# Performance work log

Hardware: AMD Instinct MI355X
Metric: run time of the kernel (lower is better)

The kernel has to match this reference:

```python
import jax, jax.numpy as jnp
import numpy as np
import math

B, C, H = 1, 3, 224
EPS = 0.05
P_INIT = 0.8
N_QUERIES = 5000


def _p_selection(it):
    # static python schedule (rescale_schedule=False)
    if 10 < it <= 50:
        return P_INIT / 2
    elif 50 < it <= 200:
        return P_INIT / 4
    elif 200 < it <= 500:
        return P_INIT / 8
    elif 500 < it <= 1000:
        return P_INIT / 16
    elif 1000 < it <= 2000:
        return P_INIT / 32
    elif 2000 < it <= 4000:
        return P_INIT / 64
    elif 4000 < it <= 6000:
        return P_INIT / 128
    elif 6000 < it <= 8000:
        return P_INIT / 256
    elif 8000 < it:
        return P_INIT / 512
    return P_INIT


def _s_schedule():
    # patch side length per iteration; pure python -> static array
    n_features = C * H * H
    return np.array(
        [max(int(round(math.sqrt(_p_selection(i) * n_features / C))), 1) for i in range(N_QUERIES)],
        dtype=np.int32,
    )


def setup_inputs() -> dict:
    key = jax.random.key(0)
    x = jax.random.uniform(key, (B, C, H, H), dtype=jnp.float32)  # image in [0,1]
    return {"x": x}


def _forward(x):
    base = jax.random.key(1)
    # init: vertical-stripe random-sign perturbation, shape [B, C, 1, H]
    k0 = jax.random.fold_in(base, 0)
    init_sign = jnp.sign(2.0 * jax.random.uniform(k0, (x.shape[0], C, 1, H), dtype=x.dtype) - 1.0)
    x_best = jnp.clip(x + EPS * init_sign, 0.0, 1.0)

    x_lo = x - EPS
    x_hi = x + EPS
    s_arr = jnp.asarray(_s_schedule())  # [N_QUERIES] int32
    idx = jnp.arange(H)

    def step(xb, si):
        s, i = si
        k = jax.random.fold_in(base, i + 1)
        k1, k2 = jax.random.split(k)
        # vh = floor(uniform * (H - s)) in {0, ..., H-s-1}
        u = jax.random.uniform(k1, (), dtype=x.dtype)
        vh = jnp.floor(u * (H - s).astype(x.dtype)).astype(jnp.int32)
        # per-channel random sign, constant over the s x s patch
        sgn = jnp.sign(2.0 * jax.random.uniform(k2, (C, 1, 1), dtype=x.dtype) - 1.0)
        # square patch mask [H, H] at offset vh with side s (mask instead of
        # dynamic-size slice assignment; jit-friendly)
        m = (idx >= vh) & (idx < vh + s)
        mask = (m[:, None] & m[None, :]).astype(x.dtype)
        xb = xb + 2.0 * EPS * sgn * mask            # broadcasts to [B, C, H, H]
        xb = jnp.clip(jnp.minimum(jnp.maximum(xb, x_lo), x_hi), 0.0, 1.0)
        return xb, None

    x_best, _ = jax.lax.scan(step, x_best, (s_arr, jnp.arange(N_QUERIES)))
    return x_best


def reference(x):
    return _forward(x)
```

## Files before the change

kernel.cpp:

```cpp
#include <hip/hip_runtime.h>
#include <stdint.h>


#define HH 224
#define NQ 5000
#define NPIX (HH * HH)
#define EPSF 0.05f

__device__ __forceinline__ void tf2x32(uint32_t k0, uint32_t k1,
                                       uint32_t x0, uint32_t x1,
                                       uint32_t& o0, uint32_t& o1) {
  uint32_t ks2 = k0 ^ k1 ^ 0x1BD11BDAu;
  x0 += k0; x1 += k1;
#define TFR(r) { x0 += x1; x1 = (x1 << (r)) | (x1 >> (32 - (r))); x1 ^= x0; }
  TFR(13) TFR(15) TFR(26) TFR(6)
  x0 += k1;  x1 += ks2 + 1u;
  TFR(17) TFR(29) TFR(16) TFR(24)
  x0 += ks2; x1 += k0 + 2u;
  TFR(13) TFR(15) TFR(26) TFR(6)
  x0 += k0;  x1 += k1 + 3u;
  TFR(17) TFR(29) TFR(16) TFR(24)
  x0 += k1;  x1 += ks2 + 4u;
  TFR(13) TFR(15) TFR(26) TFR(6)
  x0 += ks2; x1 += k0 + 5u;
#undef TFR
  o0 = x0; o1 = x1;
}

__device__ __forceinline__ int sign_from_bits(uint32_t bits) {
  uint32_t mant = bits >> 9;
  return (mant > 0x400000u) ? 1 : ((mant < 0x400000u) ? -1 : 0);
}

__device__ __forceinline__ float u01_from_bits(uint32_t bits) {
  return __uint_as_float(0x3f800000u | (bits >> 9)) - 1.0f;
}

__constant__ int SEG_LO_C[8] = {0, 11, 51, 201, 501, 1001, 2001, 4001};
__constant__ int SEG_HI_C[8] = {10, 50, 200, 500, 1000, 2000, 4000, 4999};
__constant__ int SEG_SZ_C[8] = {200, 142, 100, 71, 50, 35, 25, 18};

__global__ __launch_bounds__(512) void build_kernel(uint16_t* __restrict__ gtab,
                                                    int8_t* __restrict__ gisign) {
  int blk = blockIdx.x;
  int tid = threadIdx.x;

  if (blk == 24) {
    uint32_t g0, g1;
    tf2x32(0u, 1u, 0u, 0u, g0, g1);
    for (int i = tid; i < 3 * HH; i += 512) {
      uint32_t o0, o1;
      tf2x32(g0, g1, 0u, (uint32_t)i, o0, o1);
      gisign[i] = (int8_t)sign_from_bits(o0 ^ o1);
    }
    return;
  }

  int seg = blk / 3, c = blk % 3;
  int s = SEG_SZ_C[seg];
  __shared__ uint32_t bins[224];
  __shared__ uint16_t tab[8 * 224];
  if (tid < 224) bins[tid] = 0;
  __syncthreads();

  for (int t = SEG_LO_C[seg] + tid; t <= SEG_HI_C[seg]; t += 512) {
    uint32_t f0, f1;
    tf2x32(0u, 1u, 0u, (uint32_t)(t + 1), f0, f1);
    uint32_t a0, a1, b0, b1;
    tf2x32(f0, f1, 0u, 0u, a0, a1);
    tf2x32(f0, f1, 0u, 1u, b0, b1);
    uint32_t u0, u1;
    tf2x32(a0, a1, 0u, 0u, u0, u1);
    int vh = (int)floorf(u01_from_bits(u0 ^ u1) * (float)(HH - s));
    uint32_t c0, c1;
    tf2x32(b0, b1, 0u, (uint32_t)c, c0, c1);
    int g = sign_from_bits(c0 ^ c1);
    if (g) atomicMax(&bins[vh], (((uint32_t)(t + 1)) << 1) | (uint32_t)(g > 0));
  }
  __syncthreads();

  if (tid < 224) tab[tid] = (uint16_t)bins[tid];
  __syncthreads();
  for (int k = 1; k < 8; ++k) {
    int w = 1 << (k - 1);
    if (tid < 224) {
      uint16_t a = tab[(k - 1) * 224 + tid];
      uint16_t b = (tid + w < 224) ? tab[(k - 1) * 224 + tid + w] : (uint16_t)0;
      tab[k * 224 + tid] = (a > b) ? a : b;
    }
    __syncthreads();
  }

  const uint32_t* t32 = (const uint32_t*)tab;
  uint32_t* g32 = (uint32_t*)(gtab + (seg * 3 + c) * 1792);
  for (int i = tid; i < 896; i += 512) g32[i] = t32[i];
}

__global__ __launch_bounds__(256) void resolve_kernel(const uint16_t* __restrict__ gtab,
                                                      const int8_t* __restrict__ isign,
                                                      const float* __restrict__ x,
                                                      float* __restrict__ out) {
  int c = blockIdx.y;
  int p = blockIdx.x * 256 + threadIdx.x;
  int pi = p / HH, pj = p % HH;
  int m = min(pi, pj), M = max(pi, pj);

  const uint16_t* tc = gtab + c * 1792;

  const int SEG_S[8] = {200, 142, 100, 71, 50, 35, 25, 18};
  uint32_t best = 0;
#pragma unroll
  for (int seg = 0; seg < 8; ++seg) {
    const int s = SEG_S[seg];
    int lo = max(0, M - s + 1);
    int hi = min(m, 223 - s);
    bool ok = (lo <= hi);
    int len = ok ? (hi - lo + 1) : 1;
    int k = 31 - __clz(len);
    int o2 = hi + 1 - (1 << k);
    int b = seg * 5376 + k * 224;
    uint32_t v = max((uint32_t)tc[b + lo], (uint32_t)tc[b + o2]);
    best = max(best, ok ? v : 0u);
  }

  int sg = best ? ((best & 1u) ? 1 : -1) : (int)isign[c * HH + pj];

  int idx = c * NPIX + p;
  float xv = x[idx];
  out[idx] = (sg > 0) ? fminf(xv + EPSF, 1.0f)
           : (sg < 0) ? fmaxf(xv - EPSF, 0.0f)
                      : fminf(fmaxf(xv, 0.0f), 1.0f);
}

extern "C" void kernel_launch(void* const* d_in, const int* in_sizes, int n_in,
                              void* d_out, int out_size, void* d_ws, size_t ws_size,
                              hipStream_t stream) {
  const float* x = (const float*)d_in[0];
  float* out = (float*)d_out;
  uint16_t* gtab = (uint16_t*)d_ws;
  int8_t* gisign = (int8_t*)d_ws + 86016;

  build_kernel<<<25, 512, 0, stream>>>(gtab, gisign);
  dim3 rgrid(NPIX / 256, 3);
  resolve_kernel<<<rgrid, 256, 0, stream>>>(gtab, gisign, x, out);
}
```

Baseline: 66.09 us.

## Fuse table build and resolve into one kernel with per-block recomputation

Merges the RNG-driven table build and the per-pixel resolve into a single kernel, where every block recomputes all 5000 query draws for its channel into shared-memory bins and sparse tables. This removes the second launch, the global workspace round trip and the cross-kernel dependency. In exchange each block does the full RNG loop redundantly (about 10 serial passes per thread instead of at most 4), and uses larger shared memory, which lengthens the per-block critical path.

```diff
diff --git a/kernel.cpp b/kernel.cpp
--- a/kernel.cpp
+++ b/kernel.cpp
@@ -36,34 +36,32 @@
   return __uint_as_float(0x3f800000u | (bits >> 9)) - 1.0f;
 }
 
-__constant__ int SEG_LO_C[8] = {0, 11, 51, 201, 501, 1001, 2001, 4001};
-__constant__ int SEG_HI_C[8] = {10, 50, 200, 500, 1000, 2000, 4000, 4999};
+__device__ __forceinline__ int seg_of(int t) {
+  if (t <= 10)   return 0;
+  if (t <= 50)   return 1;
+  if (t <= 200)  return 2;
+  if (t <= 500)  return 3;
+  if (t <= 1000) return 4;
+  if (t <= 2000) return 5;
+  if (t <= 4000) return 6;
+  return 7;
+}
 __constant__ int SEG_SZ_C[8] = {200, 142, 100, 71, 50, 35, 25, 18};
 
-__global__ __launch_bounds__(512) void build_kernel(uint16_t* __restrict__ gtab,
-                                                    int8_t* __restrict__ gisign) {
+__global__ __launch_bounds__(512) void fused_kernel(const float* __restrict__ x,
+                                                    float* __restrict__ out) {
+  __shared__ uint32_t bins[8 * 224];
+  __shared__ uint16_t tab[8 * 8 * 224];
+  __shared__ int8_t isign_l[224];
   int blk = blockIdx.x;
   int tid = threadIdx.x;
+  int c = blk / 98;
+  int p = (blk - c * 98) * 512 + tid;
 
-  if (blk == 24) {
-    uint32_t g0, g1;
-    tf2x32(0u, 1u, 0u, 0u, g0, g1);
-    for (int i = tid; i < 3 * HH; i += 512) {
-      uint32_t o0, o1;
-      tf2x32(g0, g1, 0u, (uint32_t)i, o0, o1);
-      gisign[i] = (int8_t)sign_from_bits(o0 ^ o1);
-    }
-    return;
-  }
-
-  int seg = blk / 3, c = blk % 3;
-  int s = SEG_SZ_C[seg];
-  __shared__ uint32_t bins[224];
-  __shared__ uint16_t tab[8 * 224];
-  if (tid < 224) bins[tid] = 0;
+  for (int i = tid; i < 8 * 224; i += 512) bins[i] = 0;
   __syncthreads();
 
-  for (int t = SEG_LO_C[seg] + tid; t <= SEG_HI_C[seg]; t += 512) {
+  for (int t = tid; t < NQ; t += 512) {
     uint32_t f0, f1;
     tf2x32(0u, 1u, 0u, (uint32_t)(t + 1), f0, f1);
     uint32_t a0, a1, b0, b1;
@@ -71,41 +69,43 @@
     tf2x32(f0, f1, 0u, 1u, b0, b1);
     uint32_t u0, u1;
     tf2x32(a0, a1, 0u, 0u, u0, u1);
+    int seg = seg_of(t);
+    int s = SEG_SZ_C[seg];
     int vh = (int)floorf(u01_from_bits(u0 ^ u1) * (float)(HH - s));
     uint32_t c0, c1;
     tf2x32(b0, b1, 0u, (uint32_t)c, c0, c1);
     int g = sign_from_bits(c0 ^ c1);
-    if (g) atomicMax(&bins[vh], (((uint32_t)(t + 1)) << 1) | (uint32_t)(g > 0));
+    if (g) atomicMax(&bins[seg * 224 + vh],
+                     (((uint32_t)(t + 1)) << 1) | (uint32_t)(g > 0));
+  }
+
+  if (tid < 224) {
+    uint32_t g0, g1;
+    tf2x32(0u, 1u, 0u, 0u, g0, g1);
+    uint32_t o0, o1;
+    tf2x32(g0, g1, 0u, (uint32_t)(c * 224 + tid), o0, o1);
+    isign_l[tid] = (int8_t)sign_from_bits(o0 ^ o1);
   }
   __syncthreads();
 
-  if (tid < 224) tab[tid] = (uint16_t)bins[tid];
+  for (int i = tid; i < 8 * 224; i += 512) {
+    int seg = i / 224, v = i % 224;
+    tab[(seg * 8) * 224 + v] = (uint16_t)bins[i];
+  }
   __syncthreads();
   for (int k = 1; k < 8; ++k) {
     int w = 1 << (k - 1);
-    if (tid < 224) {
-      uint16_t a = tab[(k - 1) * 224 + tid];
-      uint16_t b = (tid + w < 224) ? tab[(k - 1) * 224 + tid + w] : (uint16_t)0;
-      tab[k * 224 + tid] = (a > b) ? a : b;
+    for (int i = tid; i < 8 * 224; i += 512) {
+      int seg = i / 224, v = i % 224;
+      uint16_t a = tab[(seg * 8 + k - 1) * 224 + v];
+      uint16_t b = (v + w < 224) ? tab[(seg * 8 + k - 1) * 224 + v + w] : (uint16_t)0;
+      tab[(seg * 8 + k) * 224 + v] = (a > b) ? a : b;
     }
     __syncthreads();
   }
 
-  const uint32_t* t32 = (const uint32_t*)tab;
-  uint32_t* g32 = (uint32_t*)(gtab + (seg * 3 + c) * 1792);
-  for (int i = tid; i < 896; i += 512) g32[i] = t32[i];
-}
-
-__global__ __launch_bounds__(256) void resolve_kernel(const uint16_t* __restrict__ gtab,
-                                                      const int8_t* __restrict__ isign,
-                                                      const float* __restrict__ x,
-                                                      float* __restrict__ out) {
-  int c = blockIdx.y;
-  int p = blockIdx.x * 256 + threadIdx.x;
   int pi = p / HH, pj = p % HH;
   int m = min(pi, pj), M = max(pi, pj);
-
-  const uint16_t* tc = gtab + c * 1792;
 
   const int SEG_S[8] = {200, 142, 100, 71, 50, 35, 25, 18};
   uint32_t best = 0;
@@ -118,12 +118,12 @@
     int len = ok ? (hi - lo + 1) : 1;
     int k = 31 - __clz(len);
     int o2 = hi + 1 - (1 << k);
-    int b = seg * 5376 + k * 224;
-    uint32_t v = max((uint32_t)tc[b + lo], (uint32_t)tc[b + o2]);
+    int b = (seg * 8 + k) * 224;
+    uint32_t v = max((uint32_t)tab[b + lo], (uint32_t)tab[b + o2]);
     best = max(best, ok ? v : 0u);
   }
 
-  int sg = best ? ((best & 1u) ? 1 : -1) : (int)isign[c * HH + pj];
+  int sg = best ? ((best & 1u) ? 1 : -1) : (int)isign_l[pj];
 
   int idx = c * NPIX + p;
   float xv = x[idx];
@@ -137,10 +137,5 @@
                               hipStream_t stream) {
   const float* x = (const float*)d_in[0];
   float* out = (float*)d_out;
-  uint16_t* gtab = (uint16_t*)d_ws;
-  int8_t* gisign = (int8_t*)d_ws + 86016;
-
-  build_kernel<<<25, 512, 0, stream>>>(gtab, gisign);
-  dim3 rgrid(NPIX / 256, 3);
-  resolve_kernel<<<rgrid, 256, 0, stream>>>(gtab, gisign, x, out);
+  fused_kernel<<<294, 512, 0, stream>>>(x, out);
 }
```

Result: slower. 109.7 us (+66.0%).

## Fuse table build and resolve into one kernel with flag-based spin wait

Applied to the files above, without the earlier changes.

Merges the two launches into a single 294-block kernel. The first 24 blocks build the sparse max tables and publish completion through release-stored magic flags. Every block prefetches its pixel and computes the init sign inline, then thread 0 spins on the 24 flags before the table lookups, which use atomic loads. This removes the second launch and the gap between the kernels. In exchange it depends on all blocks being resident at once, and the flags are never cleared, so later calls may not wait for the rebuilt tables.

```diff
diff --git a/kernel.cpp b/kernel.cpp
--- a/kernel.cpp
+++ b/kernel.cpp
@@ -6,6 +6,7 @@
 #define NQ 5000
 #define NPIX (HH * HH)
 #define EPSF 0.05f
+#define MAGIC 0x5EED0000u
 
 __device__ __forceinline__ void tf2x32(uint32_t k0, uint32_t k1,
                                        uint32_t x0, uint32_t x1,
@@ -40,72 +41,88 @@
 __constant__ int SEG_HI_C[8] = {10, 50, 200, 500, 1000, 2000, 4000, 4999};
 __constant__ int SEG_SZ_C[8] = {200, 142, 100, 71, 50, 35, 25, 18};
 
-__global__ __launch_bounds__(512) void build_kernel(uint16_t* __restrict__ gtab,
-                                                    int8_t* __restrict__ gisign) {
+__global__ __launch_bounds__(512) void spin_fused(const float* __restrict__ x,
+                                                  float* __restrict__ out,
+                                                  uint16_t* __restrict__ gtab,
+                                                  uint32_t* __restrict__ flags) {
+  __shared__ uint32_t bins[224];
+  __shared__ uint16_t tab[8 * 224];
+  __shared__ int ready;
   int blk = blockIdx.x;
   int tid = threadIdx.x;
 
-  if (blk == 24) {
-    uint32_t g0, g1;
-    tf2x32(0u, 1u, 0u, 0u, g0, g1);
-    for (int i = tid; i < 3 * HH; i += 512) {
-      uint32_t o0, o1;
-      tf2x32(g0, g1, 0u, (uint32_t)i, o0, o1);
-      gisign[i] = (int8_t)sign_from_bits(o0 ^ o1);
+  if (blk < 24) {
+    int seg = blk / 3, c = blk % 3;
+    int s = SEG_SZ_C[seg];
+    if (tid < 224) bins[tid] = 0;
+    __syncthreads();
+    for (int t = SEG_LO_C[seg] + tid; t <= SEG_HI_C[seg]; t += 512) {
+      uint32_t f0, f1;
+      tf2x32(0u, 1u, 0u, (uint32_t)(t + 1), f0, f1);
+      uint32_t a0, a1, b0, b1;
+      tf2x32(f0, f1, 0u, 0u, a0, a1);
+      tf2x32(f0, f1, 0u, 1u, b0, b1);
+      uint32_t u0, u1;
+      tf2x32(a0, a1, 0u, 0u, u0, u1);
+      int vh = (int)floorf(u01_from_bits(u0 ^ u1) * (float)(HH - s));
+      uint32_t c0, c1;
+      tf2x32(b0, b1, 0u, (uint32_t)c, c0, c1);
+      int g = sign_from_bits(c0 ^ c1);
+      if (g) atomicMax(&bins[vh], (((uint32_t)(t + 1)) << 1) | (uint32_t)(g > 0));
     }
-    return;
+    __syncthreads();
+    if (tid < 224) tab[tid] = (uint16_t)bins[tid];
+    __syncthreads();
+    for (int k = 1; k < 8; ++k) {
+      int w = 1 << (k - 1);
+      if (tid < 224) {
+        uint16_t a = tab[(k - 1) * 224 + tid];
+        uint16_t b = (tid + w < 224) ? tab[(k - 1) * 224 + tid + w] : (uint16_t)0;
+        tab[k * 224 + tid] = (a > b) ? a : b;
+      }
+      __syncthreads();
+    }
+    const uint32_t* t32 = (const uint32_t*)tab;
+    uint32_t* g32 = (uint32_t*)(gtab + (seg * 3 + c) * 1792);
+    for (int i = tid; i < 896; i += 512) g32[i] = t32[i];
+    __threadfence();
+    __syncthreads();
+    if (tid == 0)
+      __hip_atomic_store(&flags[blk], MAGIC + (uint32_t)blk,
+                         __ATOMIC_RELEASE, __HIP_MEMORY_SCOPE_AGENT);
   }
 
-  int seg = blk / 3, c = blk % 3;
-  int s = SEG_SZ_C[seg];
-  __shared__ uint32_t bins[224];
-  __shared__ uint16_t tab[8 * 224];
-  if (tid < 224) bins[tid] = 0;
-  __syncthreads();
+  int c = blk / 98;
+  int p = (blk - c * 98) * 512 + tid;
+  int gid = c * NPIX + p;
+  float xv = x[gid];
 
-  for (int t = SEG_LO_C[seg] + tid; t <= SEG_HI_C[seg]; t += 512) {
-    uint32_t f0, f1;
-    tf2x32(0u, 1u, 0u, (uint32_t)(t + 1), f0, f1);
-    uint32_t a0, a1, b0, b1;
-    tf2x32(f0, f1, 0u, 0u, a0, a1);
-    tf2x32(f0, f1, 0u, 1u, b0, b1);
-    uint32_t u0, u1;
-    tf2x32(a0, a1, 0u, 0u, u0, u1);
-    int vh = (int)floorf(u01_from_bits(u0 ^ u1) * (float)(HH - s));
-    uint32_t c0, c1;
-    tf2x32(b0, b1, 0u, (uint32_t)c, c0, c1);
-    int g = sign_from_bits(c0 ^ c1);
-    if (g) atomicMax(&bins[vh], (((uint32_t)(t + 1)) << 1) | (uint32_t)(g > 0));
+  int pj = p % HH;
+  int isg;
+  {
+    uint32_t g0, g1, o0, o1;
+    tf2x32(0u, 1u, 0u, 0u, g0, g1);
+    tf2x32(g0, g1, 0u, (uint32_t)(c * HH + pj), o0, o1);
+    isg = sign_from_bits(o0 ^ o1);
+  }
+
+  if (tid == 0) {
+    int good = 0;
+    for (int it = 0; it < (1 << 22) && good < 24; ++it) {
+      good = 0;
+      for (int i = 0; i < 24; ++i)
+        good += (__hip_atomic_load(&flags[i], __ATOMIC_ACQUIRE,
+                                   __HIP_MEMORY_SCOPE_AGENT) == MAGIC + (uint32_t)i);
+      if (good < 24) __builtin_amdgcn_s_sleep(8);
+    }
+    ready = 1;
   }
   __syncthreads();
+  (void)ready;
 
-  if (tid < 224) tab[tid] = (uint16_t)bins[tid];
-  __syncthreads();
-  for (int k = 1; k < 8; ++k) {
-    int w = 1 << (k - 1);
-    if (tid < 224) {
-      uint16_t a = tab[(k - 1) * 224 + tid];
-      uint16_t b = (tid + w < 224) ? tab[(k - 1) * 224 + tid + w] : (uint16_t)0;
-      tab[k * 224 + tid] = (a > b) ? a : b;
-    }
-    __syncthreads();
-  }
-
-  const uint32_t* t32 = (const uint32_t*)tab;
-  uint32_t* g32 = (uint32_t*)(gtab + (seg * 3 + c) * 1792);
-  for (int i = tid; i < 896; i += 512) g32[i] = t32[i];
-}
-
-__global__ __launch_bounds__(256) void resolve_kernel(const uint16_t* __restrict__ gtab,
-                                                      const int8_t* __restrict__ isign,
-                                                      const float* __restrict__ x,
-                                                      float* __restrict__ out) {
-  int c = blockIdx.y;
-  int p = blockIdx.x * 256 + threadIdx.x;
-  int pi = p / HH, pj = p % HH;
+  int pi = p / HH;
   int m = min(pi, pj), M = max(pi, pj);
-
-  const uint16_t* tc = gtab + c * 1792;
+  const uint32_t* gt32 = (const uint32_t*)gtab;
 
   const int SEG_S[8] = {200, 142, 100, 71, 50, 35, 25, 18};
   uint32_t best = 0;
@@ -118,16 +135,21 @@
     int len = ok ? (hi - lo + 1) : 1;
     int k = 31 - __clz(len);
     int o2 = hi + 1 - (1 << k);
-    int b = seg * 5376 + k * 224;
-    uint32_t v = max((uint32_t)tc[b + lo], (uint32_t)tc[b + o2]);
+    int e1 = c * 1792 + seg * 5376 + k * 224 + lo;
+    int e2 = c * 1792 + seg * 5376 + k * 224 + o2;
+    uint32_t w1 = __hip_atomic_load(&gt32[e1 >> 1], __ATOMIC_RELAXED,
+                                    __HIP_MEMORY_SCOPE_AGENT);
+    uint32_t w2 = __hip_atomic_load(&gt32[e2 >> 1], __ATOMIC_RELAXED,
+                                    __HIP_MEMORY_SCOPE_AGENT);
+    uint32_t v1 = (w1 >> ((e1 & 1) * 16)) & 0xFFFFu;
+    uint32_t v2 = (w2 >> ((e2 & 1) * 16)) & 0xFFFFu;
+    uint32_t v = max(v1, v2);
     best = max(best, ok ? v : 0u);
   }
 
-  int sg = best ? ((best & 1u) ? 1 : -1) : (int)isign[c * HH + pj];
+  int sg = best ? ((best & 1u) ? 1 : -1) : isg;
 
-  int idx = c * NPIX + p;
-  float xv = x[idx];
-  out[idx] = (sg > 0) ? fminf(xv + EPSF, 1.0f)
+  out[gid] = (sg > 0) ? fminf(xv + EPSF, 1.0f)
            : (sg < 0) ? fmaxf(xv - EPSF, 0.0f)
                       : fminf(fmaxf(xv, 0.0f), 1.0f);
 }
@@ -138,9 +160,7 @@
   const float* x = (const float*)d_in[0];
   float* out = (float*)d_out;
   uint16_t* gtab = (uint16_t*)d_ws;
-  int8_t* gisign = (int8_t*)d_ws + 86016;
+  uint32_t* flags = (uint32_t*)((char*)d_ws + 86016);
 
-  build_kernel<<<25, 512, 0, stream>>>(gtab, gisign);
-  dim3 rgrid(NPIX / 256, 3);
-  resolve_kernel<<<rgrid, 256, 0, stream>>>(gtab, gisign, x, out);
+  spin_fused<<<294, 512, 0, stream>>>(x, out, gtab, flags);
 }
```

Result: slower. 156.2 us (+136.3%).
